# Performance work log

Measured on AMD Instinct MI355X. Metric: run time of the kernel, lower is better.

## Reference

```python
import jax, jax.numpy as jnp
import numpy as np

B, L, D, H = 4, 2048, 1024, 16
DK = D // H  # 64


def setup_inputs() -> dict:
    key = jax.random.key(0)
    ks = jax.random.split(key, 5)
    x = jax.random.normal(ks[0], (B, L, D), dtype=jnp.float32)
    scale = 1.0 / np.sqrt(D)
    W_qkv = jax.random.normal(ks[1], (D, 3 * D), dtype=jnp.float32) * scale
    b_qkv = jnp.zeros((3 * D,), dtype=jnp.float32)
    W_out = jax.random.normal(ks[2], (D, D), dtype=jnp.float32) * scale
    b_out = jnp.zeros((D,), dtype=jnp.float32)
    return {"x": x, "W_qkv": W_qkv, "b_qkv": b_qkv, "W_out": W_out, "b_out": b_out}


def reference(x, W_qkv, b_qkv, W_out, b_out):
    Bx, Lx, Dx = x.shape
    qkv = x @ W_qkv + b_qkv                      # [B, L, 3D]
    q, k, v = jnp.split(qkv, 3, axis=-1)
    # [B, H, L, d_k]
    q = q.reshape(Bx, Lx, H, DK).transpose(0, 2, 1, 3)
    k = k.reshape(Bx, Lx, H, DK).transpose(0, 2, 1, 3)
    v = v.reshape(Bx, Lx, H, DK).transpose(0, 2, 1, 3)
    scores = jnp.einsum('bhqd,bhkd->bhqk', q, k) / np.sqrt(DK)
    causal = jnp.tril(jnp.ones((Lx, Lx), dtype=bool))
    scores = jnp.where(causal[None, None], scores, -jnp.inf)
    attn = jax.nn.softmax(scores, axis=-1)       # [B, H, L, L]
    out = jnp.einsum('bhqk,bhkd->bhqd', attn, v)
    out = out.transpose(0, 2, 1, 3).reshape(Bx, Lx, Dx)
    return out @ W_out + b_out
```

## Files before the change

### kernel.cpp

```cpp
#include <hip/hip_runtime.h>
#include <stdint.h>

#define B_ 4
#define L_ 2048
#define D_ 1024
#define H_ 16
#define DK_ 64

typedef __attribute__((ext_vector_type(8))) short bf16x8;
typedef __attribute__((ext_vector_type(4))) float f32x4;
typedef unsigned short bfu;

#define MFMA(a, b, c) __builtin_amdgcn_mfma_f32_16x16x32_bf16((a), (b), (c), 0, 0, 0)

__device__ __forceinline__ unsigned short f2bf(float f) {
  union { float f; unsigned int u; } v; v.f = f;
  unsigned int u = v.u;
  return (unsigned short)((u + 0x7fffu + ((u >> 16) & 1u)) >> 16);
}

__device__ __forceinline__ void gll16(const void* g, void* l) {
  __builtin_amdgcn_global_load_lds(
      (const __attribute__((address_space(1))) void*)g,
      (__attribute__((address_space(3))) void*)l, 16, 0, 0);
}

#define VMCNT(n_) asm volatile("s_waitcnt vmcnt(" #n_ ")" ::: "memory")
#define BARRIER() asm volatile("s_barrier" ::: "memory")


__global__ __launch_bounds__(256) void cast_x(const float* __restrict__ in,
                                              bfu* __restrict__ out, int n4) {
  int i = blockIdx.x * 256 + threadIdx.x;
  if (i >= n4) return;
  float4 v = ((const float4*)in)[i];
  ushort4 o;
  o.x = f2bf(v.x); o.y = f2bf(v.y); o.z = f2bf(v.z); o.w = f2bf(v.w);
  ((ushort4*)out)[i] = o;
}

__global__ void transpose_cast(const float* __restrict__ in, bfu* __restrict__ out,
                               int R, int C) {
  __shared__ float tile[32][33];
  int c0 = blockIdx.x * 32, r0 = blockIdx.y * 32;
  int tx = threadIdx.x, ty = threadIdx.y;
#pragma unroll
  for (int i = ty; i < 32; i += 8)
    tile[i][tx] = in[(size_t)(r0 + i) * C + c0 + tx];
  __syncthreads();
#pragma unroll
  for (int i = ty; i < 32; i += 8)
    out[(size_t)(c0 + i) * R + r0 + tx] = f2bf(tile[tx][i]);
}


template <int EPI, int BM, int BN, int WM, int WN, int OCC>
__global__ __launch_bounds__(WM * WN * 64, OCC) void gemm_s(
    const bfu* __restrict__ A, const bfu* __restrict__ Bt,
    const float* __restrict__ bias, bfu* __restrict__ Qg, bfu* __restrict__ Kg,
    bfu* __restrict__ Vtg, float* __restrict__ Out, int M, int N, int K) {
  __shared__ __align__(16) bfu LDSb[(BM + BN) * 64];
  constexpr int TH = WM * WN * 64;
  constexpr int RM = BM / WM, RN = BN / WN;
  static_assert(RM == 64 && RN == 64, "per-wave tile is 64x64");

  const int tid = threadIdx.x;
  const int lane = tid & 63;
  const int w = tid >> 6;
  const int wm = w / WN, wn = w % WN;
  const int l15 = lane & 15, l4 = lane >> 4;

  const int nwg = gridDim.x;
  const int cpx = nwg >> 3;
  const int bid = (int)blockIdx.x;
  const int swz = (bid & 7) * cpx + (bid >> 3);
  const int NTt = N / BN;
  const int m0 = ((swz & 7) + 8 * (swz / (8 * NTt))) * BM;
  const int n0 = ((swz >> 3) % NTt) * BN;

  auto stageA = [&](int t) {
    char* lb = (char*)LDSb;
#pragma unroll
    for (int j = 0; j < BM * 8 / TH; ++j) {
      int idx = j * TH + tid;
      int row = idx >> 3, c16p = idx & 7;
      int c16 = c16p ^ (row & 7);
      gll16(A + (size_t)(m0 + row) * K + t * 64 + c16 * 8,
            lb + row * 128 + c16p * 16);
    }
  };
  auto stageB = [&](int t) {
    char* lb = (char*)(LDSb + BM * 64);
#pragma unroll
    for (int j = 0; j < BN * 8 / TH; ++j) {
      int idx = j * TH + tid;
      int row = idx >> 3, c16p = idx & 7;
      int c16 = c16p ^ (row & 7);
      gll16(Bt + (size_t)(n0 + row) * K + t * 64 + c16 * 8,
            lb + row * 128 + c16p * 16);
    }
  };

  f32x4 acc[4][4] = {};
  bf16x8 af[4][2], bfh[2][2];

  auto lda = [&]() {
    const char* base = (const char*)LDSb;
#pragma unroll
    for (int mi = 0; mi < 4; ++mi)
#pragma unroll
      for (int kk = 0; kk < 2; ++kk) {
        int row = wm * RM + mi * 16 + l15;
        int ch = (kk * 4 + l4) ^ (row & 7);
        af[mi][kk] = *(const bf16x8*)(base + row * 128 + ch * 16);
      }
  };
  auto ldb = [&](int half) {
    const char* base = (const char*)(LDSb + BM * 64);
#pragma unroll
    for (int ni = 0; ni < 2; ++ni)
#pragma unroll
      for (int kk = 0; kk < 2; ++kk) {
        int row = wn * RN + half * 32 + ni * 16 + l15;
        int ch = (kk * 4 + l4) ^ (row & 7);
        bfh[ni][kk] = *(const bf16x8*)(base + row * 128 + ch * 16);
      }
  };
  auto mmh = [&](int half) {
    __builtin_amdgcn_s_setprio(1);
#pragma unroll
    for (int mi = 0; mi < 4; ++mi)
#pragma unroll
      for (int ni = 0; ni < 2; ++ni)
#pragma unroll
        for (int kk = 0; kk < 2; ++kk)
          acc[mi][half * 2 + ni] =
              MFMA(af[mi][kk], bfh[ni][kk], acc[mi][half * 2 + ni]);
    __builtin_amdgcn_s_setprio(0);
  };

  const int NT = K >> 6;
  for (int t = 0; t < NT; ++t) {
    __syncthreads();
    stageA(t); stageB(t);
    __syncthreads();
    lda();
    ldb(0); mmh(0);
    ldb(1); mmh(1);
  }

  if constexpr (EPI == 1) {
#pragma unroll
    for (int ni = 0; ni < 4; ++ni) {
      int gn = n0 + wn * RN + ni * 16 + l15;
      float bv = bias[gn];
#pragma unroll
      for (int mi = 0; mi < 4; ++mi)
#pragma unroll
        for (int rg = 0; rg < 4; ++rg) {
          int gm = m0 + wm * RM + mi * 16 + l4 * 4 + rg;
          Out[(size_t)gm * N + gn] = acc[mi][ni][rg] + bv;
        }
    }
  } else {
    const int sec = n0 >> 10;
    if (sec < 2) {
      bfu* dst = (sec == 0) ? Qg : Kg;
      const float scale = (sec == 0) ? 0.18033688011112042f : 1.0f;
#pragma unroll
      for (int ni = 0; ni < 4; ++ni) {
        int gn = n0 + wn * RN + ni * 16 + l15;
        int rem = gn & 1023;
        int hh = rem >> 6, dk = rem & 63;
        float bv = bias[gn];
#pragma unroll
        for (int mi = 0; mi < 4; ++mi)
#pragma unroll
          for (int rg = 0; rg < 4; ++rg) {
            int gm = m0 + wm * RM + mi * 16 + l4 * 4 + rg;
            int bb = gm >> 11, ll = gm & 2047;
            dst[(((size_t)(bb * H_ + hh)) * L_ + ll) * DK_ + dk] =
                f2bf((acc[mi][ni][rg] + bv) * scale);
          }
      }
    } else {
      __syncthreads();
#pragma unroll
      for (int pass = 0; pass < BN / 128; ++pass) {
        if (wn * RN >= pass * 128 && wn * RN < pass * 128 + 128) {
#pragma unroll
          for (int ni = 0; ni < 4; ++ni) {
            int n_local = wn * RN + ni * 16 + l15;
            int n_rel = n_local - pass * 128;
            int gn = n0 + n_local;
            float bv = bias[gn];
            int swzn = (n_rel & 7) << 4;
#pragma unroll
            for (int mi = 0; mi < 4; ++mi) {
              int m_base = wm * RM + mi * 16 + l4 * 4;
              int k6 = m_base & 63;
              int p0 = (m_base & ~63) |
                       ((k6 & 32) | (((k6 >> 2) & 3) << 3) | (((k6 >> 4) & 1) << 2));
              float v0 = acc[mi][ni][0] + bv, v1 = acc[mi][ni][1] + bv;
              float v2 = acc[mi][ni][2] + bv, v3 = acc[mi][ni][3] + bv;
              uint32_t w01, w23;
              asm("v_cvt_pk_bf16_f32 %0, %1, %2" : "=v"(w01) : "v"(v0), "v"(v1));
              asm("v_cvt_pk_bf16_f32 %0, %1, %2" : "=v"(w23) : "v"(v2), "v"(v3));
              *(uint32_t*)((char*)LDSb + n_rel * (BM * 2) + ((2 * p0) ^ swzn)) = w01;
              *(uint32_t*)((char*)LDSb + n_rel * (BM * 2) + ((2 * p0 + 4) ^ swzn)) = w23;
            }
          }
        }
        __syncthreads();
        if (TH >= 512 || true) {
          int n = tid >> 2;
          if (n < 128) {
            int cb = (tid & 3) * 4;
            int gnn = n0 + pass * 128 + n;
            int hh = (gnn >> 6) & 15, dk = gnn & 63;
            size_t rowbase =
                (((size_t)((m0 >> 11) * H_ + hh)) * DK_ + dk) * L_ + (m0 & 2047);
#pragma unroll
            for (int j = 0; j < 4; ++j) {
              int ch = cb + j;
              bf16x8 vv = *(const bf16x8*)((char*)LDSb + n * (BM * 2) +
                                           ((ch * 16) ^ ((n & 7) << 4)));
              *(bf16x8*)(Vtg + rowbase + ch * 8) = vv;
            }
          }
        }
        __syncthreads();
      }
    }
  }
}


__global__ __launch_bounds__(256, 3) void attn(const bfu* __restrict__ Qg,
                                               const bfu* __restrict__ Kg,
                                               const bfu* __restrict__ Vtg,
                                               bfu* __restrict__ Ao) {
  __shared__ __align__(16) bfu Ks[2 * 64 * 64];
  __shared__ __align__(16) bfu Vs[2 * 64 * 64];

  const int tid = threadIdx.x;
  const int lane = tid & 63;
  const int w = tid >> 6;
  const int l15 = lane & 15, l4 = lane >> 4;

  const int hid = blockIdx.x;
  const int xcd = hid & 7, slot = hid >> 3;
  const int bh = xcd * 8 + (slot >> 3);
  const int p = slot & 7;
  const int b = bh >> 4, h = bh & 15;

  for (int seg = 0; seg < 2; ++seg) {
    const int qb = (seg == 0) ? p : 15 - p;
    const int q0 = qb * 128;
    const int nt = 2 * qb + 2;
    const int q0w = q0 + w * 32;

    bf16x8 qf[2][2];
#pragma unroll
    for (int mi = 0; mi < 2; ++mi)
#pragma unroll
      for (int kk = 0; kk < 2; ++kk)
        qf[mi][kk] = *(const bf16x8*)(
            Qg + ((size_t)bh * L_ + q0w + mi * 16 + l15) * DK_ + kk * 32 + l4 * 8);

#pragma unroll
    for (int i = 0; i < 2; ++i) {
      int lb = i * 256 + tid;
      int r = lb >> 3, c16 = (lb & 7) ^ (r & 7);
      gll16(Kg + ((size_t)bh * L_ + r) * DK_ + c16 * 8, (char*)Ks + lb * 16);
      gll16(Vtg + ((size_t)bh * DK_ + r) * L_ + c16 * 8, (char*)Vs + lb * 16);
    }
    VMCNT(0);
    BARRIER();

    f32x4 acco[2][4] = {};
    float m[2] = {-1e30f, -1e30f};
    float l[2] = {0.f, 0.f};

    for (int t = 0; t < nt; ++t) {
      const int cur = t & 1;
      const int kv0 = t * 64;
      const char* Kc = (const char*)Ks + cur * 8192;
      const char* Vc = (const char*)Vs + cur * 8192;

      if (t + 1 < nt) {
        const int nb = (t + 1) & 1, nkv = (t + 1) * 64;
#pragma unroll
        for (int i = 0; i < 2; ++i) {
          int lb = i * 256 + tid;
          int r = lb >> 3, c16 = (lb & 7) ^ (r & 7);
          gll16(Kg + ((size_t)bh * L_ + nkv + r) * DK_ + c16 * 8,
                (char*)Ks + nb * 8192 + lb * 16);
          gll16(Vtg + ((size_t)bh * DK_ + r) * L_ + nkv + c16 * 8,
                (char*)Vs + nb * 8192 + lb * 16);
        }
        VMCNT(4);
      } else {
        VMCNT(0);
      }
      BARRIER();

      if (kv0 <= q0w + 31) {
        f32x4 s[2][4] = {};
        __builtin_amdgcn_s_setprio(1);
#pragma unroll
        for (int kk = 0; kk < 2; ++kk)
#pragma unroll
          for (int ni = 0; ni < 4; ++ni) {
            int r = ni * 16 + l15;
            int ch = (kk * 4 + l4) ^ (r & 7);
            bf16x8 kf = *(const bf16x8*)(Kc + r * 128 + ch * 16);
#pragma unroll
            for (int mi = 0; mi < 2; ++mi)
              s[mi][ni] = MFMA(kf, qf[mi][kk], s[mi][ni]);
          }
        __builtin_amdgcn_s_setprio(0);

        if (kv0 + 63 > q0w) {
#pragma unroll
          for (int mi = 0; mi < 2; ++mi) {
            int qg_ = q0w + mi * 16 + l15;
#pragma unroll
            for (int ni = 0; ni < 4; ++ni) {
              int kvg = kv0 + ni * 16 + l4 * 4;
#pragma unroll
              for (int rg = 0; rg < 4; ++rg)
                if (kvg + rg > qg_) s[mi][ni][rg] = -1e30f;
            }
          }
        }

        float mx[2];
#pragma unroll
        for (int mi = 0; mi < 2; ++mi) {
          float v = fmaxf(fmaxf(fmaxf(s[mi][0][0], s[mi][0][1]),
                                fmaxf(s[mi][0][2], s[mi][0][3])),
                          fmaxf(fmaxf(s[mi][1][0], s[mi][1][1]),
                                fmaxf(s[mi][1][2], s[mi][1][3])));
          v = fmaxf(v, fmaxf(fmaxf(fmaxf(s[mi][2][0], s[mi][2][1]),
                                   fmaxf(s[mi][2][2], s[mi][2][3])),
                             fmaxf(fmaxf(s[mi][3][0], s[mi][3][1]),
                                   fmaxf(s[mi][3][2], s[mi][3][3]))));
          v = fmaxf(v, __shfl_xor(v, 16));
          v = fmaxf(v, __shfl_xor(v, 32));
          mx[mi] = v;
        }
        float grow = fmaxf(mx[0] - m[0], mx[1] - m[1]);
        if (__any(grow > 11.0f)) {
#pragma unroll
          for (int mi = 0; mi < 2; ++mi) {
            float mn = fmaxf(m[mi], mx[mi]);
            float sc = __builtin_amdgcn_exp2f(m[mi] - mn);
            m[mi] = mn;
            l[mi] *= sc;
#pragma unroll
            for (int rg = 0; rg < 4; ++rg) {
              float scq = __shfl(sc, l4 * 4 + rg);
              acco[mi][0][rg] *= scq; acco[mi][1][rg] *= scq;
              acco[mi][2][rg] *= scq; acco[mi][3][rg] *= scq;
            }
          }
        }

        uint32_t pk[2][4][2];
#pragma unroll
        for (int mi = 0; mi < 2; ++mi)
#pragma unroll
          for (int ni = 0; ni < 4; ++ni) {
            float p0 = __builtin_amdgcn_exp2f(s[mi][ni][0] - m[mi]);
            float p1 = __builtin_amdgcn_exp2f(s[mi][ni][1] - m[mi]);
            float p2 = __builtin_amdgcn_exp2f(s[mi][ni][2] - m[mi]);
            float p3 = __builtin_amdgcn_exp2f(s[mi][ni][3] - m[mi]);
            l[mi] += (p0 + p1) + (p2 + p3);
            asm("v_cvt_pk_bf16_f32 %0, %1, %2" : "=v"(pk[mi][ni][0]) : "v"(p0), "v"(p1));
            asm("v_cvt_pk_bf16_f32 %0, %1, %2" : "=v"(pk[mi][ni][1]) : "v"(p2), "v"(p3));
          }

        __builtin_amdgcn_s_setprio(1);
#pragma unroll
        for (int kk = 0; kk < 2; ++kk) {
          union { uint32_t wd[4]; bf16x8 v; } u[2];
#pragma unroll
          for (int mi = 0; mi < 2; ++mi) {
            u[mi].wd[0] = pk[mi][2 * kk][0];
            u[mi].wd[1] = pk[mi][2 * kk][1];
            u[mi].wd[2] = pk[mi][2 * kk + 1][0];
            u[mi].wd[3] = pk[mi][2 * kk + 1][1];
          }
#pragma unroll
          for (int ni = 0; ni < 4; ++ni) {
            int r = ni * 16 + l15;
            int ch = (kk * 4 + l4) ^ (r & 7);
            bf16x8 vf = *(const bf16x8*)(Vc + r * 128 + ch * 16);
#pragma unroll
            for (int mi = 0; mi < 2; ++mi)
              acco[mi][ni] = MFMA(u[mi].v, vf, acco[mi][ni]);
          }
        }
        __builtin_amdgcn_s_setprio(0);
      }

      BARRIER();
    }

#pragma unroll
    for (int mi = 0; mi < 2; ++mi) {
      float ls = l[mi];
      ls += __shfl_xor(ls, 16);
      ls += __shfl_xor(ls, 32);
      float linv = 1.0f / ls;
#pragma unroll
      for (int rg = 0; rg < 4; ++rg) {
        float lq = __shfl(linv, l4 * 4 + rg);
        int q = q0w + mi * 16 + l4 * 4 + rg;
#pragma unroll
        for (int ni = 0; ni < 4; ++ni) {
          int d = ni * 16 + l15;
          Ao[((size_t)b * L_ + q) * D_ + h * DK_ + d] = f2bf(acco[mi][ni][rg] * lq);
        }
      }
    }
  }
}


extern "C" void kernel_launch(void* const* d_in, const int* in_sizes, int n_in,
                              void* d_out, int out_size, void* d_ws, size_t ws_size,
                              hipStream_t stream) {
  const float* x = (const float*)d_in[0];
  const float* W_qkv = (const float*)d_in[1];
  const float* b_qkv = (const float*)d_in[2];
  const float* W_out = (const float*)d_in[3];
  const float* b_out = (const float*)d_in[4];
  float* out = (float*)d_out;

  char* ws = (char*)d_ws;
  bfu* xb     = (bfu*)(ws);
  bfu* Wqkv_t = (bfu*)(ws + 16777216);
  bfu* Wout_t = (bfu*)(ws + 23068672);
  bfu* Qg     = (bfu*)(ws + 25165824);
  bfu* Kg     = (bfu*)(ws + 41943040);
  bfu* Vtg    = (bfu*)(ws + 58720256);
  bfu* Ao     = (bfu*)(ws + 75497472);

  cast_x<<<8192, 256, 0, stream>>>(x, xb, 2097152);
  transpose_cast<<<dim3(96, 32), dim3(32, 8), 0, stream>>>(W_qkv, Wqkv_t, 1024, 3072);
  transpose_cast<<<dim3(32, 32), dim3(32, 8), 0, stream>>>(W_out, Wout_t, 1024, 1024);

  gemm_s<0, 128, 256, 2, 4, 4><<<768, 512, 0, stream>>>(
      xb, Wqkv_t, b_qkv, Qg, Kg, Vtg, nullptr, 8192, 3072, 1024);
  attn<<<512, 256, 0, stream>>>(Qg, Kg, Vtg, Ao);
  gemm_s<1, 128, 128, 2, 2, 3><<<512, 256, 0, stream>>>(
      Ao, Wout_t, b_out, nullptr, nullptr, nullptr, out, 8192, 1024, 1024);
}
```

Before: 181.7 us.

## Give each GEMM wave the full M tile with fewer waves per block

Restructures the shared GEMM kernel so every wave covers all BM rows (128) and a 64-column slice, which halves the waves per workgroup (512→256 threads for QKV, 256→128 for the output projection). Each wave then reuses each B fragment across twice as many MFMAs and performs fewer LDS reads per MFMA. The cost is a doubled accumulator and A-fragment register footprint, a lower occupancy bound of 2, and fewer threads to issue global-to-LDS loads and to write out the V transpose.

```diff
diff --git a/kernel.cpp b/kernel.cpp
--- a/kernel.cpp
+++ b/kernel.cpp
@@ -54,20 +54,19 @@
 }
 
 
-template <int EPI, int BM, int BN, int WM, int WN, int OCC>
-__global__ __launch_bounds__(WM * WN * 64, OCC) void gemm_s(
+template <int EPI, int BM, int BN, int WN>
+__global__ __launch_bounds__(WN * 64, 2) void gemm_w(
     const bfu* __restrict__ A, const bfu* __restrict__ Bt,
     const float* __restrict__ bias, bfu* __restrict__ Qg, bfu* __restrict__ Kg,
     bfu* __restrict__ Vtg, float* __restrict__ Out, int M, int N, int K) {
   __shared__ __align__(16) bfu LDSb[(BM + BN) * 64];
-  constexpr int TH = WM * WN * 64;
-  constexpr int RM = BM / WM, RN = BN / WN;
-  static_assert(RM == 64 && RN == 64, "per-wave tile is 64x64");
+  constexpr int TH = WN * 64;
+  constexpr int MH = BM / 16;
+  static_assert(BN / WN == 64, "per-wave N is 64");
 
   const int tid = threadIdx.x;
   const int lane = tid & 63;
-  const int w = tid >> 6;
-  const int wm = w / WN, wn = w % WN;
+  const int wn = tid >> 6;
   const int l15 = lane & 15, l4 = lane >> 4;
 
   const int nwg = gridDim.x;
@@ -101,16 +100,16 @@
     }
   };
 
-  f32x4 acc[4][4] = {};
-  bf16x8 af[4][2], bfh[2][2];
-
-  auto lda = [&]() {
+  f32x4 acc[MH][4] = {};
+  bf16x8 af[MH][2], bh[2][2];
+
+  auto lda_all = [&]() {
     const char* base = (const char*)LDSb;
 #pragma unroll
-    for (int mi = 0; mi < 4; ++mi)
+    for (int mi = 0; mi < MH; ++mi)
 #pragma unroll
       for (int kk = 0; kk < 2; ++kk) {
-        int row = wm * RM + mi * 16 + l15;
+        int row = mi * 16 + l15;
         int ch = (kk * 4 + l4) ^ (row & 7);
         af[mi][kk] = *(const bf16x8*)(base + row * 128 + ch * 16);
       }
@@ -121,21 +120,21 @@
     for (int ni = 0; ni < 2; ++ni)
 #pragma unroll
       for (int kk = 0; kk < 2; ++kk) {
-        int row = wn * RN + half * 32 + ni * 16 + l15;
+        int row = wn * 64 + half * 32 + ni * 16 + l15;
         int ch = (kk * 4 + l4) ^ (row & 7);
-        bfh[ni][kk] = *(const bf16x8*)(base + row * 128 + ch * 16);
+        bh[ni][kk] = *(const bf16x8*)(base + row * 128 + ch * 16);
       }
   };
   auto mmh = [&](int half) {
     __builtin_amdgcn_s_setprio(1);
 #pragma unroll
-    for (int mi = 0; mi < 4; ++mi)
+    for (int mi = 0; mi < MH; ++mi)
 #pragma unroll
       for (int ni = 0; ni < 2; ++ni)
 #pragma unroll
         for (int kk = 0; kk < 2; ++kk)
           acc[mi][half * 2 + ni] =
-              MFMA(af[mi][kk], bfh[ni][kk], acc[mi][half * 2 + ni]);
+              MFMA(af[mi][kk], bh[ni][kk], acc[mi][half * 2 + ni]);
     __builtin_amdgcn_s_setprio(0);
   };
 
@@ -144,7 +143,7 @@
     __syncthreads();
     stageA(t); stageB(t);
     __syncthreads();
-    lda();
+    lda_all();
     ldb(0); mmh(0);
     ldb(1); mmh(1);
   }
@@ -152,13 +151,13 @@
   if constexpr (EPI == 1) {
 #pragma unroll
     for (int ni = 0; ni < 4; ++ni) {
-      int gn = n0 + wn * RN + ni * 16 + l15;
+      int gn = n0 + wn * 64 + ni * 16 + l15;
       float bv = bias[gn];
 #pragma unroll
-      for (int mi = 0; mi < 4; ++mi)
+      for (int mi = 0; mi < MH; ++mi)
 #pragma unroll
         for (int rg = 0; rg < 4; ++rg) {
-          int gm = m0 + wm * RM + mi * 16 + l4 * 4 + rg;
+          int gm = m0 + mi * 16 + l4 * 4 + rg;
           Out[(size_t)gm * N + gn] = acc[mi][ni][rg] + bv;
         }
     }
@@ -169,15 +168,15 @@
       const float scale = (sec == 0) ? 0.18033688011112042f : 1.0f;
 #pragma unroll
       for (int ni = 0; ni < 4; ++ni) {
-        int gn = n0 + wn * RN + ni * 16 + l15;
+        int gn = n0 + wn * 64 + ni * 16 + l15;
         int rem = gn & 1023;
         int hh = rem >> 6, dk = rem & 63;
         float bv = bias[gn];
 #pragma unroll
-        for (int mi = 0; mi < 4; ++mi)
+        for (int mi = 0; mi < MH; ++mi)
 #pragma unroll
           for (int rg = 0; rg < 4; ++rg) {
-            int gm = m0 + wm * RM + mi * 16 + l4 * 4 + rg;
+            int gm = m0 + mi * 16 + l4 * 4 + rg;
             int bb = gm >> 11, ll = gm & 2047;
             dst[(((size_t)(bb * H_ + hh)) * L_ + ll) * DK_ + dk] =
                 f2bf((acc[mi][ni][rg] + bv) * scale);
@@ -187,17 +186,17 @@
       __syncthreads();
 #pragma unroll
       for (int pass = 0; pass < BN / 128; ++pass) {
-        if (wn * RN >= pass * 128 && wn * RN < pass * 128 + 128) {
+        if (wn * 64 >= pass * 128 && wn * 64 < pass * 128 + 128) {
 #pragma unroll
           for (int ni = 0; ni < 4; ++ni) {
-            int n_local = wn * RN + ni * 16 + l15;
+            int n_local = wn * 64 + ni * 16 + l15;
             int n_rel = n_local - pass * 128;
             int gn = n0 + n_local;
             float bv = bias[gn];
             int swzn = (n_rel & 7) << 4;
 #pragma unroll
-            for (int mi = 0; mi < 4; ++mi) {
-              int m_base = wm * RM + mi * 16 + l4 * 4;
+            for (int mi = 0; mi < MH; ++mi) {
+              int m_base = mi * 16 + l4 * 4;
               int k6 = m_base & 63;
               int p0 = (m_base & ~63) |
                        ((k6 & 32) | (((k6 >> 2) & 3) << 3) | (((k6 >> 4) & 1) << 2));
@@ -212,21 +211,22 @@
           }
         }
         __syncthreads();
-        if (TH >= 512 || true) {
-          int n = tid >> 2;
-          if (n < 128) {
-            int cb = (tid & 3) * 4;
-            int gnn = n0 + pass * 128 + n;
-            int hh = (gnn >> 6) & 15, dk = gnn & 63;
-            size_t rowbase =
-                (((size_t)((m0 >> 11) * H_ + hh)) * DK_ + dk) * L_ + (m0 & 2047);
-#pragma unroll
-            for (int j = 0; j < 4; ++j) {
-              int ch = cb + j;
-              bf16x8 vv = *(const bf16x8*)((char*)LDSb + n * (BM * 2) +
-                                           ((ch * 16) ^ ((n & 7) << 4)));
-              *(bf16x8*)(Vtg + rowbase + ch * 8) = vv;
-            }
+        {
+          int n = tid / (TH / 128);
+          int cb = (tid % (TH / 128)) * (BM / 8 / (TH / 128) * 1);
+          int nch = (BM / 8) / (TH / 128);
+          int gnn = n0 + pass * 128 + n;
+          int hh = (gnn >> 6) & 15, dk = gnn & 63;
+          size_t rowbase =
+              (((size_t)((m0 >> 11) * H_ + hh)) * DK_ + dk) * L_ + (m0 & 2047);
+#pragma unroll
+          for (int j = 0; j < (BM / 8); ++j) {
+            if (j >= nch) break;
+            int ch = cb * nch / nch + (tid % (TH / 128)) * nch + j;
+            ch = (tid % (TH / 128)) * nch + j;
+            bf16x8 vv = *(const bf16x8*)((char*)LDSb + n * (BM * 2) +
+                                         ((ch * 16) ^ ((n & 7) << 4)));
+            *(bf16x8*)(Vtg + rowbase + ch * 8) = vv;
           }
         }
         __syncthreads();
@@ -452,9 +452,9 @@
   transpose_cast<<<dim3(96, 32), dim3(32, 8), 0, stream>>>(W_qkv, Wqkv_t, 1024, 3072);
   transpose_cast<<<dim3(32, 32), dim3(32, 8), 0, stream>>>(W_out, Wout_t, 1024, 1024);
 
-  gemm_s<0, 128, 256, 2, 4, 4><<<768, 512, 0, stream>>>(
+  gemm_w<0, 128, 256, 4><<<768, 256, 0, stream>>>(
       xb, Wqkv_t, b_qkv, Qg, Kg, Vtg, nullptr, 8192, 3072, 1024);
   attn<<<512, 256, 0, stream>>>(Qg, Kg, Vtg, Ao);
-  gemm_s<1, 128, 128, 2, 2, 3><<<512, 256, 0, stream>>>(
+  gemm_w<1, 128, 128, 2><<<512, 128, 0, stream>>>(
       Ao, Wout_t, b_out, nullptr, nullptr, nullptr, out, 8192, 1024, 1024);
 }
```

Measured after the change: 175.0 us. -3.7%, faster.

## Pre-pack weights into MFMA fragment layout and load B directly to registers

Applied to the files above, without the earlier changes.

Replaces the transpose-cast of the weights with a packing kernel that lays out W in MFMA B-fragment order, so each wave can load its B operands straight from global memory into registers without staging them in LDS. The GEMM is rewritten with a fixed 128x128 tile, a double-buffered A tile in LDS, and register double-buffered B loads, using vmcnt-based waits in place of full syncs. The aim is to cut LDS traffic and barriers and to overlap loads with MFMA work. In exchange, register pressure rises, the QKV GEMM now runs with smaller tiles (more blocks, more global reads of A), and the pack kernel uses uncoalesced scattered writes.

```diff
diff --git a/kernel.cpp b/kernel.cpp
--- a/kernel.cpp
+++ b/kernel.cpp
@@ -39,126 +39,116 @@
   ((ushort4*)out)[i] = o;
 }
 
-__global__ void transpose_cast(const float* __restrict__ in, bfu* __restrict__ out,
-                               int R, int C) {
-  __shared__ float tile[32][33];
-  int c0 = blockIdx.x * 32, r0 = blockIdx.y * 32;
-  int tx = threadIdx.x, ty = threadIdx.y;
-#pragma unroll
-  for (int i = ty; i < 32; i += 8)
-    tile[i][tx] = in[(size_t)(r0 + i) * C + c0 + tx];
-  __syncthreads();
-#pragma unroll
-  for (int i = ty; i < 32; i += 8)
-    out[(size_t)(c0 + i) * R + r0 + tx] = f2bf(tile[tx][i]);
-}
-
-
-template <int EPI, int BM, int BN, int WM, int WN, int OCC>
-__global__ __launch_bounds__(WM * WN * 64, OCC) void gemm_s(
-    const bfu* __restrict__ A, const bfu* __restrict__ Bt,
+__global__ __launch_bounds__(256) void wpack(const float* __restrict__ in,
+                                             bfu* __restrict__ out, int K, int C) {
+  int idx = blockIdx.x * 256 + threadIdx.x;
+  if (idx >= K * C) return;
+  int k = idx / C, c = idx % C;
+  size_t o = ((size_t)(c >> 4) * (K >> 3) + (k >> 3)) * 128 + (c & 15) * 8 + (k & 7);
+  out[o] = f2bf(in[idx]);
+}
+
+
+template <int EPI>
+__global__ __launch_bounds__(256, 2) void gemm_r(
+    const bfu* __restrict__ A, const bfu* __restrict__ Bp,
     const float* __restrict__ bias, bfu* __restrict__ Qg, bfu* __restrict__ Kg,
     bfu* __restrict__ Vtg, float* __restrict__ Out, int M, int N, int K) {
-  __shared__ __align__(16) bfu LDSb[(BM + BN) * 64];
-  constexpr int TH = WM * WN * 64;
-  constexpr int RM = BM / WM, RN = BN / WN;
-  static_assert(RM == 64 && RN == 64, "per-wave tile is 64x64");
-
+  __shared__ __align__(16) bfu As[2][128 * 64];
   const int tid = threadIdx.x;
   const int lane = tid & 63;
   const int w = tid >> 6;
-  const int wm = w / WN, wn = w % WN;
+  const int wm = w >> 1, wn = w & 1;
   const int l15 = lane & 15, l4 = lane >> 4;
 
   const int nwg = gridDim.x;
   const int cpx = nwg >> 3;
   const int bid = (int)blockIdx.x;
   const int swz = (bid & 7) * cpx + (bid >> 3);
-  const int NTt = N / BN;
-  const int m0 = ((swz & 7) + 8 * (swz / (8 * NTt))) * BM;
-  const int n0 = ((swz >> 3) % NTt) * BN;
+  const int NTt = N / 128;
+  const int m0 = ((swz & 7) + 8 * (swz / (8 * NTt))) * 128;
+  const int n0 = ((swz >> 3) % NTt) * 128;
+  const int K8 = K >> 3;
 
   auto stageA = [&](int t) {
-    char* lb = (char*)LDSb;
-#pragma unroll
-    for (int j = 0; j < BM * 8 / TH; ++j) {
-      int idx = j * TH + tid;
-      int row = idx >> 3, c16p = idx & 7;
-      int c16 = c16p ^ (row & 7);
+    char* lb = (char*)As[t & 1];
+#pragma unroll
+    for (int j = 0; j < 4; ++j) {
+      int idx = j * 256 + tid;
+      int row = idx >> 3, c16p = idx & 7, c16 = c16p ^ (row & 7);
       gll16(A + (size_t)(m0 + row) * K + t * 64 + c16 * 8,
             lb + row * 128 + c16p * 16);
     }
   };
-  auto stageB = [&](int t) {
-    char* lb = (char*)(LDSb + BM * 64);
-#pragma unroll
-    for (int j = 0; j < BN * 8 / TH; ++j) {
-      int idx = j * TH + tid;
-      int row = idx >> 3, c16p = idx & 7;
-      int c16 = c16p ^ (row & 7);
-      gll16(Bt + (size_t)(n0 + row) * K + t * 64 + c16 * 8,
-            lb + row * 128 + c16p * 16);
-    }
+
+  const size_t bbase = ((size_t)((n0 + wn * 64) >> 4)) * K8;
+  auto loadB = [&](int t, bf16x8 (&br)[4][2]) {
+#pragma unroll
+    for (int ni = 0; ni < 4; ++ni)
+#pragma unroll
+      for (int kk = 0; kk < 2; ++kk)
+        br[ni][kk] = *(const bf16x8*)(
+            Bp + (bbase + (size_t)ni * K8 + t * 8 + kk * 4 + l4) * 128 + l15 * 8);
   };
 
   f32x4 acc[4][4] = {};
-  bf16x8 af[4][2], bfh[2][2];
-
-  auto lda = [&]() {
-    const char* base = (const char*)LDSb;
+  bf16x8 af[4][2], brA[4][2], brB[4][2];
+
+  auto lda = [&](int t) {
+    const char* base = (const char*)As[t & 1];
 #pragma unroll
     for (int mi = 0; mi < 4; ++mi)
 #pragma unroll
       for (int kk = 0; kk < 2; ++kk) {
-        int row = wm * RM + mi * 16 + l15;
+        int row = wm * 64 + mi * 16 + l15;
         int ch = (kk * 4 + l4) ^ (row & 7);
         af[mi][kk] = *(const bf16x8*)(base + row * 128 + ch * 16);
       }
   };
-  auto ldb = [&](int half) {
-    const char* base = (const char*)(LDSb + BM * 64);
-#pragma unroll
-    for (int ni = 0; ni < 2; ++ni)
-#pragma unroll
-      for (int kk = 0; kk < 2; ++kk) {
-        int row = wn * RN + half * 32 + ni * 16 + l15;
-        int ch = (kk * 4 + l4) ^ (row & 7);
-        bfh[ni][kk] = *(const bf16x8*)(base + row * 128 + ch * 16);
-      }
-  };
-  auto mmh = [&](int half) {
+  auto mm_all = [&](bf16x8 (&br)[4][2]) {
     __builtin_amdgcn_s_setprio(1);
 #pragma unroll
-    for (int mi = 0; mi < 4; ++mi)
-#pragma unroll
-      for (int ni = 0; ni < 2; ++ni)
-#pragma unroll
-        for (int kk = 0; kk < 2; ++kk)
-          acc[mi][half * 2 + ni] =
-              MFMA(af[mi][kk], bfh[ni][kk], acc[mi][half * 2 + ni]);
+    for (int kk = 0; kk < 2; ++kk)
+#pragma unroll
+      for (int mi = 0; mi < 4; ++mi)
+#pragma unroll
+        for (int ni = 0; ni < 4; ++ni)
+          acc[mi][ni] = MFMA(af[mi][kk], br[ni][kk], acc[mi][ni]);
     __builtin_amdgcn_s_setprio(0);
   };
 
   const int NT = K >> 6;
-  for (int t = 0; t < NT; ++t) {
-    __syncthreads();
-    stageA(t); stageB(t);
-    __syncthreads();
-    lda();
-    ldb(0); mmh(0);
-    ldb(1); mmh(1);
+  stageA(0);
+  __builtin_amdgcn_sched_barrier(0);
+  loadB(0, brA);
+  loadB(1, brB);
+
+  for (int t = 0; t < NT; t += 2) {
+    VMCNT(8); BARRIER();
+    lda(t);
+    stageA(t + 1);
+    __builtin_amdgcn_sched_barrier(0);
+    mm_all(brA);
+    if (t + 2 < NT) loadB(t + 2, brA);
+    if (t + 2 < NT) { VMCNT(8); } else { VMCNT(0); }
+    BARRIER();
+    lda(t + 1);
+    if (t + 2 < NT) stageA(t + 2);
+    __builtin_amdgcn_sched_barrier(0);
+    mm_all(brB);
+    if (t + 3 < NT) loadB(t + 3, brB);
   }
 
   if constexpr (EPI == 1) {
 #pragma unroll
     for (int ni = 0; ni < 4; ++ni) {
-      int gn = n0 + wn * RN + ni * 16 + l15;
+      int gn = n0 + wn * 64 + ni * 16 + l15;
       float bv = bias[gn];
 #pragma unroll
       for (int mi = 0; mi < 4; ++mi)
 #pragma unroll
         for (int rg = 0; rg < 4; ++rg) {
-          int gm = m0 + wm * RM + mi * 16 + l4 * 4 + rg;
+          int gm = m0 + wm * 64 + mi * 16 + l4 * 4 + rg;
           Out[(size_t)gm * N + gn] = acc[mi][ni][rg] + bv;
         }
     }
@@ -169,7 +159,7 @@
       const float scale = (sec == 0) ? 0.18033688011112042f : 1.0f;
 #pragma unroll
       for (int ni = 0; ni < 4; ++ni) {
-        int gn = n0 + wn * RN + ni * 16 + l15;
+        int gn = n0 + wn * 64 + ni * 16 + l15;
         int rem = gn & 1023;
         int hh = rem >> 6, dk = rem & 63;
         float bv = bias[gn];
@@ -177,7 +167,7 @@
         for (int mi = 0; mi < 4; ++mi)
 #pragma unroll
           for (int rg = 0; rg < 4; ++rg) {
-            int gm = m0 + wm * RM + mi * 16 + l4 * 4 + rg;
+            int gm = m0 + wm * 64 + mi * 16 + l4 * 4 + rg;
             int bb = gm >> 11, ll = gm & 2047;
             dst[(((size_t)(bb * H_ + hh)) * L_ + ll) * DK_ + dk] =
                 f2bf((acc[mi][ni][rg] + bv) * scale);
@@ -186,50 +176,39 @@
     } else {
       __syncthreads();
 #pragma unroll
-      for (int pass = 0; pass < BN / 128; ++pass) {
-        if (wn * RN >= pass * 128 && wn * RN < pass * 128 + 128) {
-#pragma unroll
-          for (int ni = 0; ni < 4; ++ni) {
-            int n_local = wn * RN + ni * 16 + l15;
-            int n_rel = n_local - pass * 128;
-            int gn = n0 + n_local;
-            float bv = bias[gn];
-            int swzn = (n_rel & 7) << 4;
-#pragma unroll
-            for (int mi = 0; mi < 4; ++mi) {
-              int m_base = wm * RM + mi * 16 + l4 * 4;
-              int k6 = m_base & 63;
-              int p0 = (m_base & ~63) |
-                       ((k6 & 32) | (((k6 >> 2) & 3) << 3) | (((k6 >> 4) & 1) << 2));
-              float v0 = acc[mi][ni][0] + bv, v1 = acc[mi][ni][1] + bv;
-              float v2 = acc[mi][ni][2] + bv, v3 = acc[mi][ni][3] + bv;
-              uint32_t w01, w23;
-              asm("v_cvt_pk_bf16_f32 %0, %1, %2" : "=v"(w01) : "v"(v0), "v"(v1));
-              asm("v_cvt_pk_bf16_f32 %0, %1, %2" : "=v"(w23) : "v"(v2), "v"(v3));
-              *(uint32_t*)((char*)LDSb + n_rel * (BM * 2) + ((2 * p0) ^ swzn)) = w01;
-              *(uint32_t*)((char*)LDSb + n_rel * (BM * 2) + ((2 * p0 + 4) ^ swzn)) = w23;
-            }
-          }
-        }
-        __syncthreads();
-        if (TH >= 512 || true) {
-          int n = tid >> 2;
-          if (n < 128) {
-            int cb = (tid & 3) * 4;
-            int gnn = n0 + pass * 128 + n;
-            int hh = (gnn >> 6) & 15, dk = gnn & 63;
-            size_t rowbase =
-                (((size_t)((m0 >> 11) * H_ + hh)) * DK_ + dk) * L_ + (m0 & 2047);
-#pragma unroll
-            for (int j = 0; j < 4; ++j) {
-              int ch = cb + j;
-              bf16x8 vv = *(const bf16x8*)((char*)LDSb + n * (BM * 2) +
-                                           ((ch * 16) ^ ((n & 7) << 4)));
-              *(bf16x8*)(Vtg + rowbase + ch * 8) = vv;
-            }
-          }
-        }
-        __syncthreads();
+      for (int ni = 0; ni < 4; ++ni) {
+        int n_local = wn * 64 + ni * 16 + l15;
+        int gn = n0 + n_local;
+        float bv = bias[gn];
+        int swzn = (n_local & 7) << 4;
+#pragma unroll
+        for (int mi = 0; mi < 4; ++mi) {
+          int m_base = wm * 64 + mi * 16 + l4 * 4;
+          int k6 = m_base & 63;
+          int p0 = (m_base & ~63) |
+                   ((k6 & 32) | (((k6 >> 2) & 3) << 3) | (((k6 >> 4) & 1) << 2));
+          float v0 = acc[mi][ni][0] + bv, v1 = acc[mi][ni][1] + bv;
+          float v2 = acc[mi][ni][2] + bv, v3 = acc[mi][ni][3] + bv;
+          uint32_t w01, w23;
+          asm("v_cvt_pk_bf16_f32 %0, %1, %2" : "=v"(w01) : "v"(v0), "v"(v1));
+          asm("v_cvt_pk_bf16_f32 %0, %1, %2" : "=v"(w23) : "v"(v2), "v"(v3));
+          *(uint32_t*)((char*)As + n_local * 256 + ((2 * p0) ^ swzn)) = w01;
+          *(uint32_t*)((char*)As + n_local * 256 + ((2 * p0 + 4) ^ swzn)) = w23;
+        }
+      }
+      __syncthreads();
+      int n = tid >> 1;
+      int cb = (tid & 1) * 8;
+      int gnn = n0 + n;
+      int hh = (gnn >> 6) & 15, dk = gnn & 63;
+      size_t rowbase =
+          (((size_t)((m0 >> 11) * H_ + hh)) * DK_ + dk) * L_ + (m0 & 2047);
+#pragma unroll
+      for (int j = 0; j < 8; ++j) {
+        int ch = cb + j;
+        bf16x8 vv = *(const bf16x8*)((char*)As + n * 256 +
+                                     ((ch * 16) ^ ((n & 7) << 4)));
+        *(bf16x8*)(Vtg + rowbase + ch * 8) = vv;
       }
     }
   }
@@ -441,20 +420,20 @@
 
   char* ws = (char*)d_ws;
   bfu* xb     = (bfu*)(ws);
-  bfu* Wqkv_t = (bfu*)(ws + 16777216);
-  bfu* Wout_t = (bfu*)(ws + 23068672);
+  bfu* Wqkv_p = (bfu*)(ws + 16777216);
+  bfu* Wout_p = (bfu*)(ws + 23068672);
   bfu* Qg     = (bfu*)(ws + 25165824);
   bfu* Kg     = (bfu*)(ws + 41943040);
   bfu* Vtg    = (bfu*)(ws + 58720256);
   bfu* Ao     = (bfu*)(ws + 75497472);
 
   cast_x<<<8192, 256, 0, stream>>>(x, xb, 2097152);
-  transpose_cast<<<dim3(96, 32), dim3(32, 8), 0, stream>>>(W_qkv, Wqkv_t, 1024, 3072);
-  transpose_cast<<<dim3(32, 32), dim3(32, 8), 0, stream>>>(W_out, Wout_t, 1024, 1024);
-
-  gemm_s<0, 128, 256, 2, 4, 4><<<768, 512, 0, stream>>>(
-      xb, Wqkv_t, b_qkv, Qg, Kg, Vtg, nullptr, 8192, 3072, 1024);
+  wpack<<<12288, 256, 0, stream>>>(W_qkv, Wqkv_p, 1024, 3072);
+  wpack<<<4096, 256, 0, stream>>>(W_out, Wout_p, 1024, 1024);
+
+  gemm_r<0><<<1536, 256, 0, stream>>>(xb, Wqkv_p, b_qkv, Qg, Kg, Vtg, nullptr,
+                                      8192, 3072, 1024);
   attn<<<512, 256, 0, stream>>>(Qg, Kg, Vtg, Ao);
-  gemm_s<1, 128, 128, 2, 2, 3><<<512, 256, 0, stream>>>(
-      Ao, Wout_t, b_out, nullptr, nullptr, nullptr, out, 8192, 1024, 1024);
-}
+  gemm_r<1><<<512, 256, 0, stream>>>(Ao, Wout_p, b_out, nullptr, nullptr, nullptr,
+                                     out, 8192, 1024, 1024);
+}
```

New measurement: 163.9 us. 1.11x faster.
